# Kernel tuning notes

Hardware: AMD Instinct MI355X
Metric: run time of the kernel (lower is better)

## Reference

```python
import jax, jax.numpy as jnp
import numpy as np


def positional_encoding(n_tokens, d_model, dtype=jnp.float32):
    # standard sinusoidal PE: pe[pos, 2i] = sin(pos / 10000^(2i/d)), pe[pos, 2i+1] = cos(...)
    pos = jnp.arange(n_tokens, dtype=dtype)[:, None]            # [n, 1]
    i = jnp.arange(0, d_model, 2, dtype=dtype)[None, :]         # [1, d/2]
    angle = pos / jnp.power(jnp.asarray(10000.0, dtype), i / d_model)
    pe = jnp.zeros((n_tokens, d_model), dtype)
    pe = pe.at[:, 0::2].set(jnp.sin(angle))
    pe = pe.at[:, 1::2].set(jnp.cos(angle))
    return pe


def layer_norm(x, gamma, beta, eps=1e-5):
    mu = jnp.mean(x, axis=-1, keepdims=True)
    var = jnp.var(x, axis=-1, keepdims=True)
    return (x - mu) * jax.lax.rsqrt(var + eps) * gamma + beta


def setup_inputs() -> dict:
    key = jax.random.key(0)
    ks = jax.random.split(key, 4)
    b, n, d = 4, 1024, 1024
    dh = 1024  # dim_hidden_linear
    s = 1.0 / np.sqrt(d)
    return {
        "token_embedding": jax.random.normal(ks[0], (b, n, d), jnp.float32),
        "ln_gamma": jnp.ones((d,), jnp.float32),
        "ln_beta": jnp.zeros((d,), jnp.float32),
        "Wq": jax.random.normal(ks[1], (d, dh), jnp.float32) * s,
        "bq": jnp.zeros((dh,), jnp.float32),
        "Wk": jax.random.normal(ks[2], (d, dh), jnp.float32) * s,
        "bk": jnp.zeros((dh,), jnp.float32),
        "Wv": jax.random.normal(ks[3], (d, dh), jnp.float32) * s,
        "bv": jnp.zeros((dh,), jnp.float32),
        "num_heads": 16,
    }


def reference(token_embedding, ln_gamma, ln_beta, Wq, bq, Wk, bk, Wv, bv, num_heads):
    b, n, d = token_embedding.shape
    pe = positional_encoding(n, d)                      # [n, d]
    x = token_embedding + pe[None, :, :]                # broadcast over batch
    x = layer_norm(x, ln_gamma, ln_beta)
    q = x @ Wq + bq                                     # [b, n, dh]
    k = x @ Wk + bk
    v = x @ Wv + bv
    dh = q.shape[-1]
    hd = dh // num_heads                                # per-head dim
    q = q.reshape(b, n, num_heads, hd)
    k = k.reshape(b, n, num_heads, hd)
    v = v.reshape(b, n, num_heads, hd)
    scale = 1.0 / jnp.sqrt(jnp.asarray(hd, q.dtype))
    scores = jnp.einsum("bqhd,bkhd->bhqk", q, k) * scale  # [b, h, n, n]
    attn = jax.nn.softmax(scores, axis=-1)
    out = jnp.einsum("bhqk,bkhd->bqhd", attn, v)          # [b, n, h, hd]
    return out.reshape(b, n, dh)
```

## Files before the change

### kernel.cpp

```cpp
#include <hip/hip_runtime.h>
#include <hip/hip_bf16.h>
#include <math.h>

typedef __attribute__((ext_vector_type(8))) short bf16x8;
typedef __attribute__((ext_vector_type(4))) short bf16x4;
typedef __attribute__((ext_vector_type(4))) float f32x4;

static __device__ __forceinline__ void gld16(const void* g, void* l) {
    __builtin_amdgcn_global_load_lds(
        (const __attribute__((address_space(1))) unsigned int*)g,
        (__attribute__((address_space(3))) unsigned int*)l, 16, 0, 0);
}

static __device__ __forceinline__ short f2bf_s(float f) {
    __hip_bfloat16 h = __float2bfloat16(f);
    short s;
    __builtin_memcpy(&s, &h, 2);
    return s;
}

__global__ __launch_bounds__(256) void peln_wt_kernel(
    const float* __restrict__ emb,
    const float* __restrict__ gamma,
    const float* __restrict__ beta,
    const float* __restrict__ Wq,
    const float* __restrict__ Wk,
    const float* __restrict__ Wv,
    __hip_bfloat16* __restrict__ x,
    __hip_bfloat16* __restrict__ Wt)
{
    const int tid = threadIdx.x;
    if (blockIdx.x < 4096) {
        const int row = blockIdx.x;
        const int t   = row & 1023;
        float4 e = ((const float4*)(emb + (size_t)row * 1024))[tid];
        float v[4] = {e.x, e.y, e.z, e.w};
        float s = 0.f, ss = 0.f;
        #pragma unroll
        for (int kk = 0; kk < 4; ++kk) {
            int c = tid * 4 + kk;
            float ang = (float)t * exp2f(-13.287712379549449f * (float)(c >> 1) * (1.0f / 512.0f));
            float pe  = (c & 1) ? __cosf(ang) : __sinf(ang);
            v[kk] += pe;
            s  += v[kk];
            ss += v[kk] * v[kk];
        }
        #pragma unroll
        for (int off = 1; off < 64; off <<= 1) {
            s  += __shfl_xor(s, off);
            ss += __shfl_xor(ss, off);
        }
        __shared__ float red_s[4], red_ss[4];
        int wave = tid >> 6, lane = tid & 63;
        if (lane == 0) { red_s[wave] = s; red_ss[wave] = ss; }
        __syncthreads();
        float S  = red_s[0] + red_s[1] + red_s[2] + red_s[3];
        float SS = red_ss[0] + red_ss[1] + red_ss[2] + red_ss[3];
        float mu   = S * (1.0f / 1024.0f);
        float var  = SS * (1.0f / 1024.0f) - mu * mu;
        float rstd = rsqrtf(var + 1e-5f);
        #pragma unroll
        for (int kk = 0; kk < 4; ++kk) {
            int c = tid * 4 + kk;
            float y = (v[kk] - mu) * rstd * gamma[c] + beta[c];
            x[(size_t)row * 1024 + c] = __float2bfloat16(y);
        }
    } else {
        __shared__ __hip_bfloat16 tile[32][33];
        int wid = blockIdx.x - 4096;
        int zz  = wid >> 10;
        int rem = wid & 1023;
        int bx = rem & 31, by = rem >> 5;
        int tx = tid & 31, ty = tid >> 5;
        const float* src = (zz == 0) ? Wq : (zz == 1) ? Wk : Wv;
        __hip_bfloat16* dst = Wt + (size_t)zz * 1024 * 1024;
        int x0 = bx * 32, y0 = by * 32;
        #pragma unroll
        for (int kk = 0; kk < 4; ++kk)
            tile[ty + 8 * kk][tx] =
                __float2bfloat16(src[(size_t)(y0 + ty + 8 * kk) * 1024 + x0 + tx]);
        __syncthreads();
        #pragma unroll
        for (int kk = 0; kk < 4; ++kk)
            dst[(size_t)(x0 + ty + 8 * kk) * 1024 + y0 + tx] = tile[tx][ty + 8 * kk];
    }
}

__global__ __launch_bounds__(256) void qkv_gemm(
    const __hip_bfloat16* __restrict__ X,
    const __hip_bfloat16* __restrict__ Wt,
    const float* __restrict__ bq,
    const float* __restrict__ bk,
    const float* __restrict__ bv,
    __hip_bfloat16* __restrict__ qkv,
    __hip_bfloat16* __restrict__ vt)
{
    union SMem {
        struct { __hip_bfloat16 A[128 * 64]; __hip_bfloat16 B[128 * 64]; } s;
        __hip_bfloat16 C[128 * 132];
    };
    __shared__ __align__(16) SMem sm;

    const int id   = blockIdx.x;
    const int xcd  = id & 7;
    const int rest = id >> 3;
    const int j    = rest % 3;
    const int mblk = rest / 3;
    const int m0   = mblk * 128;
    const int n0   = (xcd * 3 + j) * 128;
    const int t    = n0 >> 10;
    const int nn0  = n0 & 1023;
    const __hip_bfloat16* W = Wt + (size_t)t * 1024 * 1024;

    const int tid  = threadIdx.x;
    const int wave = tid >> 6, lane = tid & 63;
    const int wm = wave & 1, wn = wave >> 1;
    const int lm = lane & 15, quad = lane >> 4;

    const int srow = lane >> 3;
    const int skc  = ((lane & 7) ^ srow) * 8;
    const int rbase = wave * 32;
    const __hip_bfloat16* gA = X + (size_t)(m0 + rbase + srow) * 1024 + skc;
    const __hip_bfloat16* gB = W + (size_t)(nn0 + rbase + srow) * 1024 + skc;
    __hip_bfloat16* lA = sm.s.A + rbase * 64;
    __hip_bfloat16* lB = sm.s.B + rbase * 64;

    f32x4 acc[4][4];
    #pragma unroll
    for (int i = 0; i < 4; ++i)
        #pragma unroll
        for (int jj = 0; jj < 4; ++jj)
            acc[i][jj] = (f32x4){0.f, 0.f, 0.f, 0.f};

    #pragma unroll
    for (int n = 0; n < 4; ++n) {
        gld16(gA + (size_t)n * 8 * 1024, lA + n * 8 * 64);
        gld16(gB + (size_t)n * 8 * 1024, lB + n * 8 * 64);
    }

    for (int k0 = 0; k0 < 1024; k0 += 64) {
        __syncthreads();

        bf16x8 a[2][4], b[2][4];
        #pragma unroll
        for (int ks = 0; ks < 2; ++ks) {
            #pragma unroll
            for (int i = 0; i < 4; ++i) {
                int row = wm * 64 + i * 16 + lm;
                a[ks][i] = *(const bf16x8*)(sm.s.A + (size_t)row * 64
                                            + (((ks * 4 + quad) ^ (lm & 7)) * 8));
            }
            #pragma unroll
            for (int jj = 0; jj < 4; ++jj) {
                int row = wn * 64 + jj * 16 + lm;
                b[ks][jj] = *(const bf16x8*)(sm.s.B + (size_t)row * 64
                                             + (((ks * 4 + quad) ^ (lm & 7)) * 8));
            }
        }
        __syncthreads();

        if (k0 + 64 < 1024) {
            #pragma unroll
            for (int n = 0; n < 4; ++n) {
                gld16(gA + (size_t)n * 8 * 1024 + k0 + 64, lA + n * 8 * 64);
                gld16(gB + (size_t)n * 8 * 1024 + k0 + 64, lB + n * 8 * 64);
            }
        }

        #pragma unroll
        for (int ks = 0; ks < 2; ++ks)
            #pragma unroll
            for (int i = 0; i < 4; ++i)
                #pragma unroll
                for (int jj = 0; jj < 4; ++jj)
                    acc[i][jj] = __builtin_amdgcn_mfma_f32_16x16x32_bf16(a[ks][i], b[ks][jj], acc[i][jj], 0, 0, 0);
    }

    const float* bias = (t == 0) ? bq : (t == 1) ? bk : bv;
    if (t < 2) {
        #pragma unroll
        for (int jj = 0; jj < 4; ++jj) {
            int col = wn * 64 + jj * 16 + lm;
            float bb = bias[nn0 + col];
            #pragma unroll
            for (int i = 0; i < 4; ++i)
                #pragma unroll
                for (int r = 0; r < 4; ++r) {
                    int row = wm * 64 + i * 16 + quad * 4 + r;
                    sm.C[(size_t)row * 132 + col] = __float2bfloat16(acc[i][jj][r] + bb);
                }
        }
        __syncthreads();
        __hip_bfloat16* out = qkv + (size_t)t * 4096 * 1024;
        #pragma unroll
        for (int c = 0; c < 8; ++c) {
            int g = tid + 256 * c;
            int row = g >> 4;
            int colc = (g & 15) * 8;
            bf16x8 vch = *(const bf16x8*)&sm.C[(size_t)row * 132 + colc];
            *(bf16x8*)(out + (size_t)(m0 + row) * 1024 + nn0 + colc) = vch;
        }
    } else {
        #pragma unroll
        for (int jj = 0; jj < 4; ++jj) {
            int col = wn * 64 + jj * 16 + lm;
            float bb = bias[nn0 + col];
            #pragma unroll
            for (int i = 0; i < 4; ++i)
                #pragma unroll
                for (int r = 0; r < 4; ++r) {
                    int row = wm * 64 + i * 16 + quad * 4 + r;
                    sm.C[(size_t)col * 132 + row] = __float2bfloat16(acc[i][jj][r] + bb);
                }
        }
        __syncthreads();
        const int bbase = (m0 >> 10) * 16 + (nn0 >> 6);
        const int mloc  = m0 & 1023;
        #pragma unroll
        for (int c = 0; c < 8; ++c) {
            int g = tid + 256 * c;
            int col = g >> 4;
            int rch = (g & 15) * 8;
            bf16x8 vch = *(const bf16x8*)&sm.C[(size_t)col * 132 + rch];
            int bh = bbase + (col >> 6);
            int d  = col & 63;
            *(bf16x8*)(vt + ((size_t)bh * 64 + d) * 1024 + mloc + rch) = vch;
        }
    }
}

__global__ __launch_bounds__(256, 2) void attn_kernel(
    const __hip_bfloat16* __restrict__ q,
    const __hip_bfloat16* __restrict__ k,
    const __hip_bfloat16* __restrict__ vt,
    float* __restrict__ out)
{
    __shared__ __align__(16) __hip_bfloat16 Kbuf[2][128 * 64];
    __shared__ __align__(16) __hip_bfloat16 Vbuf[2][2][64 * 64];
    __shared__ short ldsPT[4][32 * 64];
    const int id   = blockIdx.x;
    const int bh   = (id & 7) * 8 + ((id >> 3) & 7);
    const int qblk = id >> 6;
    const int b = bh >> 4, h = bh & 15;
    const int wave = threadIdx.x >> 6, lane = threadIdx.x & 63;
    const int lm = lane & 15, quad = lane >> 4;
    const int qbase = qblk * 128 + wave * 32;
    const float CEXP = 0.18033688011112042f;

    bf16x8 bqf[2][2];
    #pragma unroll
    for (int i = 0; i < 2; ++i)
        #pragma unroll
        for (int ks = 0; ks < 2; ++ks)
            bqf[i][ks] = *(const bf16x8*)(q + (size_t)(b * 1024 + qbase + 16 * i + lm) * 1024
                                            + h * 64 + ks * 32 + quad * 8);

    const __hip_bfloat16* kg = k + (size_t)(b * 1024) * 1024 + h * 64;
    const __hip_bfloat16* vg = vt + (size_t)bh * 64 * 1024;
    const int srow = lane >> 3;
    const int skc  = ((lane & 7) ^ srow) * 8;

    f32x4 OT[4][2];
    float li[2] = {0.f, 0.f};
    #pragma unroll
    for (int nt = 0; nt < 4; ++nt)
        #pragma unroll
        for (int i = 0; i < 2; ++i)
            OT[nt][i] = (f32x4){0.f, 0.f, 0.f, 0.f};

    auto stageKV = [&](int buf, int kt) {
        #pragma unroll
        for (int n = 0; n < 4; ++n) {
            int r0 = wave * 32 + n * 8;
            gld16(kg + (size_t)(kt + r0 + srow) * 1024 + skc, Kbuf[buf] + r0 * 64);
        }
        int half = wave >> 1;
        #pragma unroll
        for (int n = 0; n < 4; ++n) {
            int d0 = (wave & 1) * 32 + n * 8;
            gld16(vg + (size_t)(d0 + srow) * 1024 + kt + half * 64 + skc,
                  Vbuf[buf][half] + d0 * 64);
        }
    };

    stageKV(0, 0);

    for (int tt = 0; tt < 8; ++tt) {
        __syncthreads();
        if (tt + 1 < 8) stageKV((tt + 1) & 1, (tt + 1) * 128);

        const __hip_bfloat16* Kb = Kbuf[tt & 1];

        #pragma unroll
        for (int sr = 0; sr < 2; ++sr) {
            const __hip_bfloat16* Vb = Vbuf[tt & 1][sr];
            bf16x8 ak[4][2], av[4][2];
            #pragma unroll
            for (int jt = 0; jt < 4; ++jt)
                #pragma unroll
                for (int ks = 0; ks < 2; ++ks)
                    ak[jt][ks] = *(const bf16x8*)(Kb + (size_t)(sr * 64 + 16 * jt + lm) * 64
                                                  + (((ks * 4 + quad) ^ (lm & 7)) * 8));
            #pragma unroll
            for (int nt = 0; nt < 4; ++nt)
                #pragma unroll
                for (int ks = 0; ks < 2; ++ks)
                    av[nt][ks] = *(const bf16x8*)(Vb + (size_t)(16 * nt + lm) * 64
                                                  + (((ks * 4 + quad) ^ (lm & 7)) * 8));

            f32x4 ST[2][4];
            #pragma unroll
            for (int i = 0; i < 2; ++i)
                #pragma unroll
                for (int jt = 0; jt < 4; ++jt)
                    ST[i][jt] = (f32x4){0.f, 0.f, 0.f, 0.f};
            #pragma unroll
            for (int ks = 0; ks < 2; ++ks)
                #pragma unroll
                for (int i = 0; i < 2; ++i)
                    #pragma unroll
                    for (int jt = 0; jt < 4; ++jt)
                        ST[i][jt] = __builtin_amdgcn_mfma_f32_16x16x32_bf16(ak[jt][ks], bqf[i][ks], ST[i][jt], 0, 0, 0);

            #pragma unroll
            for (int i = 0; i < 2; ++i)
                #pragma unroll
                for (int jt = 0; jt < 4; ++jt) {
                    bf16x4 pk;
                    #pragma unroll
                    for (int r = 0; r < 4; ++r) {
                        float p = __builtin_amdgcn_exp2f(ST[i][jt][r] * CEXP);
                        li[i] += p;
                        pk[r] = f2bf_s(p);
                    }
                    int u = jt * 2 + (quad >> 1);
                    *(bf16x4*)&ldsPT[wave][(16 * i + lm) * 64
                        + ((u ^ (lm & 7)) << 3) + (quad & 1) * 4] = pk;
                }

            bf16x8 bp[2][2];
            #pragma unroll
            for (int i = 0; i < 2; ++i)
                #pragma unroll
                for (int ks = 0; ks < 2; ++ks)
                    bp[i][ks] = *(const bf16x8*)&ldsPT[wave][(16 * i + lm) * 64
                        + (((ks * 4 + quad) ^ (lm & 7)) << 3)];
            #pragma unroll
            for (int ks = 0; ks < 2; ++ks)
                #pragma unroll
                for (int nt = 0; nt < 4; ++nt)
                    #pragma unroll
                    for (int i = 0; i < 2; ++i)
                        OT[nt][i] = __builtin_amdgcn_mfma_f32_16x16x32_bf16(av[nt][ks], bp[i][ks], OT[nt][i], 0, 0, 0);
        }
    }

    #pragma unroll
    for (int i = 0; i < 2; ++i) {
        li[i] += __shfl_xor(li[i], 16);
        li[i] += __shfl_xor(li[i], 32);
    }

    #pragma unroll
    for (int i = 0; i < 2; ++i) {
        float inv = 1.0f / li[i];
        int qrow = qbase + 16 * i + lm;
        #pragma unroll
        for (int nt = 0; nt < 4; ++nt) {
            float4 o4 = {OT[nt][i][0] * inv, OT[nt][i][1] * inv,
                         OT[nt][i][2] * inv, OT[nt][i][3] * inv};
            *(float4*)(out + (size_t)(b * 1024 + qrow) * 1024 + h * 64 + 16 * nt + quad * 4) = o4;
        }
    }
}

extern "C" void kernel_launch(void* const* d_in, const int* in_sizes, int n_in,
                              void* d_out, int out_size, void* d_ws, size_t ws_size,
                              hipStream_t stream)
{
    const float* emb   = (const float*)d_in[0];
    const float* gamma = (const float*)d_in[1];
    const float* beta  = (const float*)d_in[2];
    const float* Wq    = (const float*)d_in[3];
    const float* bq    = (const float*)d_in[4];
    const float* Wk    = (const float*)d_in[5];
    const float* bk    = (const float*)d_in[6];
    const float* Wv    = (const float*)d_in[7];
    const float* bv    = (const float*)d_in[8];
    float* out = (float*)d_out;

    __hip_bfloat16* ws  = (__hip_bfloat16*)d_ws;
    __hip_bfloat16* x   = ws;
    __hip_bfloat16* Wt  = x   + (size_t)4096 * 1024;
    __hip_bfloat16* qkv = Wt  + (size_t)3 * 1024 * 1024;
    __hip_bfloat16* vt  = qkv + (size_t)2 * 4096 * 1024;

    peln_wt_kernel<<<4096 + 3072, 256, 0, stream>>>(emb, gamma, beta, Wq, Wk, Wv, x, Wt);
    qkv_gemm<<<768, 256, 0, stream>>>(x, Wt, bq, bk, bv, qkv, vt);
    attn_kernel<<<512, 256, 0, stream>>>(qkv, qkv + (size_t)4096 * 1024, vt, out);
}
```

Before: 149.9 us.

## Switch attention to 32x32x16 MFMA with register-resident P via permlane32 swap

Rewrites the attention inner loop to use 32x32x16 bf16 MFMA tiles instead of 16x16x32, so each wave computes its 32 query rows against 32-key tiles. The softmax probabilities are packed with v_cvt_pk_bf16_f32 and rearranged across lane halves with v_permlane32_swap, which removes the per-wave LDS round trip (ldsPT store plus reload) for the P operand. This cuts LDS traffic and fragment loads, and per the public docs larger MFMA tiles have higher operand reuse. The cost is larger accumulator register tiles, which may pressure occupancy, plus reliance on gfx950-specific inline asm.

```diff
diff --git a/kernel.cpp b/kernel.cpp
--- a/kernel.cpp
+++ b/kernel.cpp
@@ -3,8 +3,8 @@
 #include <math.h>
 
 typedef __attribute__((ext_vector_type(8))) short bf16x8;
-typedef __attribute__((ext_vector_type(4))) short bf16x4;
 typedef __attribute__((ext_vector_type(4))) float f32x4;
+typedef __attribute__((ext_vector_type(16))) float f32x16;
 
 static __device__ __forceinline__ void gld16(const void* g, void* l) {
     __builtin_amdgcn_global_load_lds(
@@ -12,11 +12,10 @@
         (__attribute__((address_space(3))) unsigned int*)l, 16, 0, 0);
 }
 
-static __device__ __forceinline__ short f2bf_s(float f) {
-    __hip_bfloat16 h = __float2bfloat16(f);
-    short s;
-    __builtin_memcpy(&s, &h, 2);
-    return s;
+static __device__ __forceinline__ unsigned cvtpk(float lo, float hi) {
+    unsigned r;
+    asm("v_cvt_pk_bf16_f32 %0, %1, %2" : "=v"(r) : "v"(lo), "v"(hi));
+    return r;
 }
 
 __global__ __launch_bounds__(256) void peln_wt_kernel(
@@ -237,36 +236,33 @@
 {
     __shared__ __align__(16) __hip_bfloat16 Kbuf[2][128 * 64];
     __shared__ __align__(16) __hip_bfloat16 Vbuf[2][2][64 * 64];
-    __shared__ short ldsPT[4][32 * 64];
     const int id   = blockIdx.x;
     const int bh   = (id & 7) * 8 + ((id >> 3) & 7);
     const int qblk = id >> 6;
     const int b = bh >> 4, h = bh & 15;
     const int wave = threadIdx.x >> 6, lane = threadIdx.x & 63;
-    const int lm = lane & 15, quad = lane >> 4;
+    const int l31 = lane & 31, hi5 = lane >> 5;
     const int qbase = qblk * 128 + wave * 32;
     const float CEXP = 0.18033688011112042f;
 
-    bf16x8 bqf[2][2];
-    #pragma unroll
-    for (int i = 0; i < 2; ++i)
-        #pragma unroll
-        for (int ks = 0; ks < 2; ++ks)
-            bqf[i][ks] = *(const bf16x8*)(q + (size_t)(b * 1024 + qbase + 16 * i + lm) * 1024
-                                            + h * 64 + ks * 32 + quad * 8);
+    bf16x8 bq32[4];
+    #pragma unroll
+    for (int slab = 0; slab < 4; ++slab)
+        bq32[slab] = *(const bf16x8*)(q + (size_t)(b * 1024 + qbase + l31) * 1024
+                                        + h * 64 + (slab * 2 + hi5) * 8);
 
     const __hip_bfloat16* kg = k + (size_t)(b * 1024) * 1024 + h * 64;
     const __hip_bfloat16* vg = vt + (size_t)bh * 64 * 1024;
     const int srow = lane >> 3;
     const int skc  = ((lane & 7) ^ srow) * 8;
 
-    f32x4 OT[4][2];
-    float li[2] = {0.f, 0.f};
-    #pragma unroll
-    for (int nt = 0; nt < 4; ++nt)
-        #pragma unroll
-        for (int i = 0; i < 2; ++i)
-            OT[nt][i] = (f32x4){0.f, 0.f, 0.f, 0.f};
+    f32x16 OT[2];
+    #pragma unroll
+    for (int dt = 0; dt < 2; ++dt)
+        #pragma unroll
+        for (int r = 0; r < 16; ++r)
+            OT[dt][r] = 0.f;
+    float li = 0.f;
 
     auto stageKV = [&](int buf, int kt) {
         #pragma unroll
@@ -294,84 +290,70 @@
         #pragma unroll
         for (int sr = 0; sr < 2; ++sr) {
             const __hip_bfloat16* Vb = Vbuf[tt & 1][sr];
-            bf16x8 ak[4][2], av[4][2];
-            #pragma unroll
-            for (int jt = 0; jt < 4; ++jt)
-                #pragma unroll
-                for (int ks = 0; ks < 2; ++ks)
-                    ak[jt][ks] = *(const bf16x8*)(Kb + (size_t)(sr * 64 + 16 * jt + lm) * 64
-                                                  + (((ks * 4 + quad) ^ (lm & 7)) * 8));
-            #pragma unroll
-            for (int nt = 0; nt < 4; ++nt)
-                #pragma unroll
-                for (int ks = 0; ks < 2; ++ks)
-                    av[nt][ks] = *(const bf16x8*)(Vb + (size_t)(16 * nt + lm) * 64
-                                                  + (((ks * 4 + quad) ^ (lm & 7)) * 8));
-
-            f32x4 ST[2][4];
-            #pragma unroll
-            for (int i = 0; i < 2; ++i)
-                #pragma unroll
-                for (int jt = 0; jt < 4; ++jt)
-                    ST[i][jt] = (f32x4){0.f, 0.f, 0.f, 0.f};
-            #pragma unroll
-            for (int ks = 0; ks < 2; ++ks)
-                #pragma unroll
-                for (int i = 0; i < 2; ++i)
-                    #pragma unroll
-                    for (int jt = 0; jt < 4; ++jt)
-                        ST[i][jt] = __builtin_amdgcn_mfma_f32_16x16x32_bf16(ak[jt][ks], bqf[i][ks], ST[i][jt], 0, 0, 0);
-
-            #pragma unroll
-            for (int i = 0; i < 2; ++i)
-                #pragma unroll
-                for (int jt = 0; jt < 4; ++jt) {
-                    bf16x4 pk;
-                    #pragma unroll
-                    for (int r = 0; r < 4; ++r) {
-                        float p = __builtin_amdgcn_exp2f(ST[i][jt][r] * CEXP);
-                        li[i] += p;
-                        pk[r] = f2bf_s(p);
-                    }
-                    int u = jt * 2 + (quad >> 1);
-                    *(bf16x4*)&ldsPT[wave][(16 * i + lm) * 64
-                        + ((u ^ (lm & 7)) << 3) + (quad & 1) * 4] = pk;
-                }
-
-            bf16x8 bp[2][2];
-            #pragma unroll
-            for (int i = 0; i < 2; ++i)
-                #pragma unroll
-                for (int ks = 0; ks < 2; ++ks)
-                    bp[i][ks] = *(const bf16x8*)&ldsPT[wave][(16 * i + lm) * 64
-                        + (((ks * 4 + quad) ^ (lm & 7)) << 3)];
-            #pragma unroll
-            for (int ks = 0; ks < 2; ++ks)
-                #pragma unroll
-                for (int nt = 0; nt < 4; ++nt)
-                    #pragma unroll
-                    for (int i = 0; i < 2; ++i)
-                        OT[nt][i] = __builtin_amdgcn_mfma_f32_16x16x32_bf16(av[nt][ks], bp[i][ks], OT[nt][i], 0, 0, 0);
-        }
-    }
-
-    #pragma unroll
-    for (int i = 0; i < 2; ++i) {
-        li[i] += __shfl_xor(li[i], 16);
-        li[i] += __shfl_xor(li[i], 32);
-    }
-
-    #pragma unroll
-    for (int i = 0; i < 2; ++i) {
-        float inv = 1.0f / li[i];
-        int qrow = qbase + 16 * i + lm;
-        #pragma unroll
-        for (int nt = 0; nt < 4; ++nt) {
-            float4 o4 = {OT[nt][i][0] * inv, OT[nt][i][1] * inv,
-                         OT[nt][i][2] * inv, OT[nt][i][3] * inv};
-            *(float4*)(out + (size_t)(b * 1024 + qrow) * 1024 + h * 64 + 16 * nt + quad * 4) = o4;
-        }
-    }
+
+            f32x16 ST[2];
+            #pragma unroll
+            for (int kt = 0; kt < 2; ++kt) {
+                #pragma unroll
+                for (int r = 0; r < 16; ++r) ST[kt][r] = 0.f;
+                #pragma unroll
+                for (int slab = 0; slab < 4; ++slab) {
+                    bf16x8 ak = *(const bf16x8*)(Kb
+                        + (size_t)(sr * 64 + kt * 32 + l31) * 64
+                        + (((slab * 2 + hi5) ^ (l31 & 7)) * 8));
+                    ST[kt] = __builtin_amdgcn_mfma_f32_32x32x16_bf16(ak, bq32[slab], ST[kt], 0, 0, 0);
+                }
+            }
+
+            unsigned pw[4][4];
+            #pragma unroll
+            for (int kt = 0; kt < 2; ++kt) {
+                float pv[16];
+                #pragma unroll
+                for (int r = 0; r < 16; ++r) {
+                    pv[r] = __builtin_amdgcn_exp2f(ST[kt][r] * CEXP);
+                    li += pv[r];
+                }
+                #pragma unroll
+                for (int s = 0; s < 2; ++s) {
+                    unsigned P0 = cvtpk(pv[8 * s + 0], pv[8 * s + 1]);
+                    unsigned P1 = cvtpk(pv[8 * s + 2], pv[8 * s + 3]);
+                    unsigned P2 = cvtpk(pv[8 * s + 4], pv[8 * s + 5]);
+                    unsigned P3 = cvtpk(pv[8 * s + 6], pv[8 * s + 7]);
+                    asm("v_permlane32_swap_b32 %0, %1" : "+v"(P0), "+v"(P2));
+                    asm("v_permlane32_swap_b32 %0, %1" : "+v"(P1), "+v"(P3));
+                    int ks = kt * 2 + s;
+                    pw[ks][0] = P0; pw[ks][1] = P1; pw[ks][2] = P2; pw[ks][3] = P3;
+                }
+            }
+
+            #pragma unroll
+            for (int dt = 0; dt < 2; ++dt)
+                #pragma unroll
+                for (int ks = 0; ks < 4; ++ks) {
+                    bf16x8 av = *(const bf16x8*)(Vb
+                        + (size_t)(dt * 32 + l31) * 64
+                        + (((ks * 2 + hi5) ^ (l31 & 7)) * 8));
+                    bf16x8 pf;
+                    __builtin_memcpy(&pf, pw[ks], 16);
+                    OT[dt] = __builtin_amdgcn_mfma_f32_32x32x16_bf16(av, pf, OT[dt], 0, 0, 0);
+                }
+        }
+    }
+
+    li += __shfl_xor(li, 32);
+    float inv = 1.0f / li;
+    const int qrow = qbase + l31;
+
+    #pragma unroll
+    for (int dt = 0; dt < 2; ++dt)
+        #pragma unroll
+        for (int g = 0; g < 4; ++g) {
+            float4 o4 = {OT[dt][4 * g + 0] * inv, OT[dt][4 * g + 1] * inv,
+                         OT[dt][4 * g + 2] * inv, OT[dt][4 * g + 3] * inv};
+            *(float4*)(out + (size_t)(b * 1024 + qrow) * 1024
+                       + h * 64 + dt * 32 + 8 * g + 4 * hi5) = o4;
+        }
 }
 
 extern "C" void kernel_launch(void* const* d_in, const int* in_sizes, int n_in,
```

Measured after the change: 149.7 us. No clear change (-0.1%).
